# Performance work log

Hardware: AMD Instinct MI355X
Metric: run time of the kernel (lower is better)

The kernel has to match this reference:

```python
import jax, jax.numpy as jnp
import numpy as np
import math

B, S, D = 2, 2048, 1024
H = 16
HD = D // H
FFN = 2048
E = 8
TOP_K = 2
CAP_FACTOR = 1.25
EPS = 1e-6
BASE = 10000.0
CAP = max(math.ceil(B * S * TOP_K * CAP_FACTOR / E), 1)  # 1280


def setup_inputs() -> dict:
    key = jax.random.key(0)
    ks = jax.random.split(key, 6)
    sd = 0.02
    return {
        "x": jax.random.normal(ks[0], (B, S, D), jnp.float32),
        "g1": jnp.ones((D,), jnp.float32),
        "w_qkv": jax.random.normal(ks[1], (D, 3 * D), jnp.float32) * sd,
        "w_o": jax.random.normal(ks[2], (D, D), jnp.float32) * sd,
        "g2": jnp.ones((D,), jnp.float32),
        "w_router": jax.random.normal(ks[3], (D, E), jnp.float32) * sd,
        "w1": jax.random.normal(ks[4], (E, D, FFN), jnp.float32) * sd,
        "w2": jax.random.normal(ks[5], (E, FFN, D), jnp.float32) * sd,
    }


def _rmsnorm(x, w):
    rms = jax.lax.rsqrt(jnp.mean(x * x, axis=-1, keepdims=True) + EPS)
    return w * x * rms


def _rope(x, cos, sin):
    # x: [b,h,s,hd]; consecutive pairs (2i, 2i+1) form complex numbers
    xr = x[..., 0::2]
    xi = x[..., 1::2]
    c = cos[None, None]  # [1,1,s,hd/2]
    s_ = sin[None, None]
    out_r = xr * c - xi * s_
    out_i = xr * s_ + xi * c
    return jnp.stack([out_r, out_i], axis=-1).reshape(x.shape)


def _mha(x, w_qkv, w_o):
    b, s, d = x.shape
    qkv = x @ w_qkv
    q, k, v = jnp.split(qkv, 3, axis=-1)
    to_heads = lambda z: z.reshape(b, s, H, HD).transpose(0, 2, 1, 3)
    q, k, v = to_heads(q), to_heads(k), to_heads(v)
    # rotary embedding
    theta = BASE ** (-2.0 * (jnp.arange(HD // 2, dtype=jnp.float32) / HD))
    freqs = jnp.arange(s, dtype=jnp.float32)[:, None] * theta[None, :]  # [s,hd/2]
    cos, sin = jnp.cos(freqs), jnp.sin(freqs)
    q = _rope(q, cos, sin)
    k = _rope(k, cos, sin)
    scores = jnp.einsum('bhqd,bhkd->bhqk', q, k) / jnp.sqrt(jnp.float32(HD))
    causal = jnp.tril(jnp.ones((s, s), dtype=bool))
    scores = jnp.where(causal, scores, -jnp.inf)
    attn = jax.nn.softmax(scores, axis=-1)
    y = jnp.einsum('bhqk,bhkd->bhqd', attn, v)
    y = y.transpose(0, 2, 1, 3).reshape(b, s, d)
    return y @ w_o


def _moe(x, w_router, w1, w2):
    b, s, d = x.shape
    t = b * s
    xf = x.reshape(t, d)
    logits = xf.astype(jnp.float32) @ w_router.astype(jnp.float32)
    probs = jax.nn.softmax(logits, axis=-1)  # [t,E]
    g, eidx = jax.lax.top_k(probs, TOP_K)  # [t,K]
    fg = g.reshape(t * TOP_K)
    fe = eidx.reshape(t * TOP_K)
    tok_of = jnp.arange(t * TOP_K) // TOP_K
    # per-expert masked gates, then capacity-based top-CAP selection
    masked = jnp.where(fe[None, :] == jnp.arange(E)[:, None], fg[None, :], -jnp.inf)  # [E, t*K]
    vals, idx = jax.lax.top_k(masked, CAP)  # [E, CAP]
    valid = jnp.isfinite(vals)
    gates = jnp.where(valid, vals, 0.0)  # dropped/empty slots get zero gate
    tok = tok_of[idx]  # [E, CAP] token ids (arbitrary for invalid slots, gate 0)
    xe = xf[tok]  # [E, CAP, d]
    h = jax.nn.relu(jnp.einsum('ecd,edf->ecf', xe, w1))
    ye = jnp.einsum('ecf,efd->ecd', h, w2) * gates[..., None]
    y = jnp.zeros_like(xf).at[tok.reshape(-1)].add(ye.reshape(-1, d))
    return y.reshape(b, s, d)


def reference(x, g1, w_qkv, w_o, g2, w_router, w1, w2):
    x = x + _mha(_rmsnorm(x, g1), w_qkv, w_o)
    x = x + _moe(_rmsnorm(x, g2), w_router, w1, w2)
    return x
```

## Files before the change

kernel.cpp:

```cpp
#include <hip/hip_runtime.h>
#include <math.h>


#define B_   2
#define S_   2048
#define D_   1024
#define H_   16
#define HD_  64
#define FFN_ 2048
#define E_   8
#define CAP_ 1280
#define T_   (B_*S_)

typedef unsigned short u16;
typedef __attribute__((ext_vector_type(8))) short     short8;
typedef __attribute__((ext_vector_type(8))) _Float16  half8;
typedef __attribute__((ext_vector_type(8))) unsigned short ushort8v;
typedef __attribute__((ext_vector_type(4))) float     f32x4;

__device__ __forceinline__ u16 f2bf(float f) {
  unsigned u = __float_as_uint(f);
  return (u16)((u + 0x7fffu + ((u >> 16) & 1u)) >> 16);
}
__device__ __forceinline__ float bf2f(u16 h) {
  return __uint_as_float(((unsigned)h) << 16);
}
__device__ __forceinline__ u16 f2h(float f) {
  _Float16 h = (_Float16)f;
  return __builtin_bit_cast(u16, h);
}
__device__ __forceinline__ float h2f(u16 b) {
  return (float)__builtin_bit_cast(_Float16, b);
}

__device__ __forceinline__ void cstore(float* p, float v) { *p = v; }
__device__ __forceinline__ void cstore(u16* p, float v)   { *p = f2bf(v); }

__device__ __forceinline__ void glds16(const u16* g, u16* l) {
  __builtin_amdgcn_global_load_lds(
      (const __attribute__((address_space(1))) unsigned int*)g,
      (__attribute__((address_space(3))) unsigned int*)l, 16, 0, 0);
}

__global__ void init_k(int* cnt) {
  if (threadIdx.x < 16) cnt[threadIdx.x] = 0;
}

__global__ __launch_bounds__(256) void rmsnorm_k(const float* __restrict__ x,
                                                 const float* __restrict__ g,
                                                 float* __restrict__ of,
                                                 u16*   __restrict__ ob,
                                                 u16*   __restrict__ ohh,
                                                 u16*   __restrict__ ohl) {
  const int t = blockIdx.x, tid = threadIdx.x;
  const float4 xv = ((const float4*)(x + (size_t)t * D_))[tid];
  float ss = xv.x*xv.x + xv.y*xv.y + xv.z*xv.z + xv.w*xv.w;
  #pragma unroll
  for (int off = 32; off; off >>= 1) ss += __shfl_down(ss, off);
  __shared__ float wsum[4];
  if ((tid & 63) == 0) wsum[tid >> 6] = ss;
  __syncthreads();
  const float tot = wsum[0] + wsum[1] + wsum[2] + wsum[3];
  const float rms = 1.0f / sqrtf(tot * (1.0f / D_) + 1e-6f);
  const float4 gv = ((const float4*)g)[tid];
  float4 o;
  o.x = gv.x * xv.x * rms;
  o.y = gv.y * xv.y * rms;
  o.z = gv.z * xv.z * rms;
  o.w = gv.w * xv.w * rms;
  if (of) ((float4*)(of + (size_t)t * D_))[tid] = o;
  if (ob) {
    ushort4 h;
    h.x = f2bf(o.x); h.y = f2bf(o.y); h.z = f2bf(o.z); h.w = f2bf(o.w);
    ((ushort4*)(ob + (size_t)t * D_))[tid] = h;
  }
  if (ohh) {
    ushort4 hh, hl;
    hh.x = f2h(o.x); hl.x = f2h(o.x - h2f(hh.x));
    hh.y = f2h(o.y); hl.y = f2h(o.y - h2f(hh.y));
    hh.z = f2h(o.z); hl.z = f2h(o.z - h2f(hh.z));
    hh.w = f2h(o.w); hl.w = f2h(o.w - h2f(hh.w));
    ((ushort4*)(ohh + (size_t)t * D_))[tid] = hh;
    ((ushort4*)(ohl + (size_t)t * D_))[tid] = hl;
  }
}

template<bool RESID>
__global__ __launch_bounds__(256) void gemm_split(const u16* __restrict__ Ah,
                                                  const u16* __restrict__ Al,
                                                  const u16* __restrict__ Bh,
                                                  const u16* __restrict__ Bl,
                                                  const float* __restrict__ resid,
                                                  float* __restrict__ C,
                                                  int K, int lda, int ldb, int ldc) {
  __shared__ u16 AsH[128 * 32], AsL[128 * 32];
  __shared__ u16 BsH[128 * 32], BsL[128 * 32];
  const int tid = threadIdx.x;
  const int bm = blockIdx.y, bn = blockIdx.x;
  const int lane = tid & 63, wave = tid >> 6;
  const int wy = wave >> 1, wx = wave & 1;
  const int l15 = lane & 15, lq = lane >> 4;
  f32x4 acc[4][4];
  #pragma unroll
  for (int i = 0; i < 4; ++i)
    #pragma unroll
    for (int j = 0; j < 4; ++j)
      #pragma unroll
      for (int r = 0; r < 4; ++r) acc[i][j][r] = 0.0f;
  const int srow = lane >> 2, skc = (lane & 3) * 8;
  size_t ga[2], gb[2];
  int ldsoff[2];
  #pragma unroll
  for (int c = 0; c < 2; ++c) {
    const int q = wave * 2 + c;
    ga[c] = (size_t)(bm * 128 + q * 16 + srow) * lda + skc;
    gb[c] = (size_t)(bn * 128 + q * 16 + srow) * ldb + skc;
    ldsoff[c] = q * 512 + lane * 8;
  }

  for (int kt = 0; kt < K; kt += 32) {
    __syncthreads();
    #pragma unroll
    for (int c = 0; c < 2; ++c) {
      glds16(Ah + ga[c] + kt, &AsH[ldsoff[c]]);
      glds16(Al + ga[c] + kt, &AsL[ldsoff[c]]);
      glds16(Bh + gb[c] + kt, &BsH[ldsoff[c]]);
      glds16(Bl + gb[c] + kt, &BsL[ldsoff[c]]);
    }
    __syncthreads();
    half8 ah[4], al[4], bh[4], bl[4];
    #pragma unroll
    for (int i = 0; i < 4; ++i) {
      const int row = (wy * 64 + i * 16 + l15) * 32 + lq * 8;
      ah[i] = *(const half8*)&AsH[row];
      al[i] = *(const half8*)&AsL[row];
    }
    #pragma unroll
    for (int j = 0; j < 4; ++j) {
      const int row = (wx * 64 + j * 16 + l15) * 32 + lq * 8;
      bh[j] = *(const half8*)&BsH[row];
      bl[j] = *(const half8*)&BsL[row];
    }
    #pragma unroll
    for (int i = 0; i < 4; ++i)
      #pragma unroll
      for (int j = 0; j < 4; ++j) {
        acc[i][j] = __builtin_amdgcn_mfma_f32_16x16x32_f16(ah[i], bh[j], acc[i][j], 0, 0, 0);
        acc[i][j] = __builtin_amdgcn_mfma_f32_16x16x32_f16(ah[i], bl[j], acc[i][j], 0, 0, 0);
        acc[i][j] = __builtin_amdgcn_mfma_f32_16x16x32_f16(al[i], bh[j], acc[i][j], 0, 0, 0);
      }
  }
  #pragma unroll
  for (int i = 0; i < 4; ++i)
    #pragma unroll
    for (int j = 0; j < 4; ++j)
      #pragma unroll
      for (int r = 0; r < 4; ++r) {
        const int row = bm * 128 + wy * 64 + i * 16 + lq * 4 + r;
        const int col = bn * 128 + wx * 64 + j * 16 + l15;
        float v = acc[i][j][r];
        if (RESID) v += resid[(size_t)row * ldc + col];
        C[(size_t)row * ldc + col] = v;
      }
}

__global__ __launch_bounds__(256) void wsplit_t_k(const float* __restrict__ src,
                                                  u16* __restrict__ dh,
                                                  u16* __restrict__ dl,
                                                  int R, int C) {
  __shared__ float tile[32][33];
  const int tid = threadIdx.x;
  const int r0 = blockIdx.y * 32, c0 = blockIdx.x * 32;
  const int tx = tid & 31, ty = tid >> 5;
  #pragma unroll
  for (int i = 0; i < 4; ++i)
    tile[ty + i * 8][tx] = src[(size_t)(r0 + ty + i * 8) * C + c0 + tx];
  __syncthreads();
  #pragma unroll
  for (int i = 0; i < 4; ++i) {
    const float v = tile[tx][ty + i * 8];
    const u16 hh = f2h(v);
    const size_t o = (size_t)(c0 + ty + i * 8) * R + r0 + tx;
    dh[o] = hh;
    dl[o] = f2h(v - h2f(hh));
  }
}

__global__ __launch_bounds__(256) void ropesplit_k(const float* __restrict__ qkv,
                                                   u16* __restrict__ qhi, u16* __restrict__ qlo,
                                                   u16* __restrict__ khi, u16* __restrict__ klo) {
  const int i = blockIdx.x * 256 + threadIdx.x;
  const int j = i & 31;
  const int h = (i >> 5) & 15;
  const int t = i >> 9;
  const int s = t & (S_ - 1);
  const int b = t >> 11;
  const int bh = b * 16 + h;
  const float theta = (float)pow(10000.0, -(double)j / 32.0);
  const float fr = (float)s * theta;
  const float c = cosf(fr), sn = sinf(fr);
  const float2 q = *(const float2*)(qkv + (size_t)t * 3072 + h * 64 + 2 * j);
  const float2 k = *(const float2*)(qkv + (size_t)t * 3072 + 1024 + h * 64 + 2 * j);
  const float q0 = (q.x * c - q.y * sn) * 0.125f;
  const float q1 = (q.x * sn + q.y * c) * 0.125f;
  const float k0 = k.x * c - k.y * sn;
  const float k1 = k.x * sn + k.y * c;
  const size_t o = ((size_t)bh * S_ + s) * 32 + j;
  const u16 qh0 = f2bf(q0), qh1 = f2bf(q1);
  const u16 kh0 = f2bf(k0), kh1 = f2bf(k1);
  ((unsigned*)qhi)[o] = (unsigned)qh0 | ((unsigned)qh1 << 16);
  ((unsigned*)khi)[o] = (unsigned)kh0 | ((unsigned)kh1 << 16);
  const u16 ql0 = f2bf(q0 - bf2f(qh0)), ql1 = f2bf(q1 - bf2f(qh1));
  const u16 kl0 = f2bf(k0 - bf2f(kh0)), kl1 = f2bf(k1 - bf2f(kh1));
  ((unsigned*)qlo)[o] = (unsigned)ql0 | ((unsigned)ql1 << 16);
  ((unsigned*)klo)[o] = (unsigned)kl0 | ((unsigned)kl1 << 16);
}

__global__ __launch_bounds__(256) void vsplit_k(const float* __restrict__ qkv,
                                                u16* __restrict__ vthi,
                                                u16* __restrict__ vtlo) {
  __shared__ float tile[64][65];
  const int st = blockIdx.x, bh = blockIdx.y;
  const int b = bh >> 4, h = bh & 15;
  const int tid = threadIdx.x;
  const int c = tid & 63, r4 = tid >> 6;
  #pragma unroll
  for (int i = 0; i < 16; ++i) {
    const int r = i * 4 + r4;
    tile[r][c] = qkv[(size_t)(b * S_ + st * 64 + r) * 3072 + 2048 + h * 64 + c];
  }
  __syncthreads();
  #pragma unroll
  for (int i = 0; i < 16; ++i) {
    const int d = i * 4 + r4;
    const float v = tile[c][d];
    const u16 hi = f2bf(v);
    const size_t o = ((size_t)bh * 64 + d) * S_ + st * 64 + c;
    vthi[o] = hi;
    vtlo[o] = f2bf(v - bf2f(hi));
  }
}

__global__ __launch_bounds__(256) void attn_mfma_k(const u16* __restrict__ qhi,
                                                   const u16* __restrict__ qlo,
                                                   const u16* __restrict__ khi,
                                                   const u16* __restrict__ klo,
                                                   const u16* __restrict__ vthi,
                                                   const u16* __restrict__ vtlo,
                                                   u16* __restrict__ ahh,
                                                   u16* __restrict__ ahl,
                                                   float* __restrict__ PO,
                                                   float* __restrict__ Pm,
                                                   float* __restrict__ Pl2) {
  __shared__ u16 Kh[64 * 68], Kl[64 * 68];
  __shared__ u16 Vh[64 * 68], Vl[64 * 68];
  __shared__ u16 Ph[4][16 * 68], Pl[4][16 * 68];
  const int tid = threadIdx.x, lane = tid & 63, wave = tid >> 6;
  const int bi = blockIdx.x;
  int qt, k0, k1, chunk;
  bool partial;
  if (bi < 32) {
    qt = 31 - (bi >> 1); chunk = bi & 1;
    const int nk = qt + 1, cut = nk >> 1;
    k0 = chunk ? cut : 0;
    k1 = chunk ? nk : cut;
    partial = true;
  } else {
    qt = 47 - bi; chunk = 0; k0 = 0; k1 = qt + 1; partial = false;
  }
  const int bh = blockIdx.y;
  const int l15 = lane & 15, lq = lane >> 4;
  const size_t hb = (size_t)bh * S_ * 64;
  const int qrow = qt * 64 + wave * 16 + l15;
  short8 qh[2], ql[2];
  qh[0] = *(const short8*)(qhi + hb + (size_t)qrow * 64 + lq * 8);
  qh[1] = *(const short8*)(qhi + hb + (size_t)qrow * 64 + 32 + lq * 8);
  ql[0] = *(const short8*)(qlo + hb + (size_t)qrow * 64 + lq * 8);
  ql[1] = *(const short8*)(qlo + hb + (size_t)qrow * 64 + 32 + lq * 8);
  f32x4 O[4];
  float m_i[4], l_i[4];
  #pragma unroll
  for (int n = 0; n < 4; ++n)
    #pragma unroll
    for (int r = 0; r < 4; ++r) O[n][r] = 0.0f;
  #pragma unroll
  for (int r = 0; r < 4; ++r) { m_i[r] = -__builtin_inff(); l_i[r] = 0.0f; }

  for (int kt = k0; kt < k1; ++kt) {
    __syncthreads();
    #pragma unroll
    for (int it = 0; it < 2; ++it) {
      const int idx = it * 256 + tid;
      const int row = idx >> 3, c8 = (idx & 7) * 8;
      const size_t koff = hb + (size_t)(kt * 64 + row) * 64 + c8;
      *(ushort8v*)&Kh[row * 68 + c8] = *(const ushort8v*)(khi + koff);
      *(ushort8v*)&Kl[row * 68 + c8] = *(const ushort8v*)(klo + koff);
      const size_t voff = ((size_t)bh * 64 + row) * S_ + kt * 64 + c8;
      *(ushort8v*)&Vh[row * 68 + c8] = *(const ushort8v*)(vthi + voff);
      *(ushort8v*)&Vl[row * 68 + c8] = *(const ushort8v*)(vtlo + voff);
    }
    __syncthreads();
    f32x4 sc[4];
    #pragma unroll
    for (int n = 0; n < 4; ++n)
      #pragma unroll
      for (int r = 0; r < 4; ++r) sc[n][r] = 0.0f;
    #pragma unroll
    for (int n = 0; n < 4; ++n) {
      const int krow = (n * 16 + l15) * 68 + lq * 8;
      const short8 kb0 = *(const short8*)&Kh[krow];
      const short8 kb1 = *(const short8*)&Kh[krow + 32];
      const short8 kl0 = *(const short8*)&Kl[krow];
      const short8 kl1 = *(const short8*)&Kl[krow + 32];
      sc[n] = __builtin_amdgcn_mfma_f32_16x16x32_bf16(qh[0], kb0, sc[n], 0, 0, 0);
      sc[n] = __builtin_amdgcn_mfma_f32_16x16x32_bf16(qh[1], kb1, sc[n], 0, 0, 0);
      sc[n] = __builtin_amdgcn_mfma_f32_16x16x32_bf16(qh[0], kl0, sc[n], 0, 0, 0);
      sc[n] = __builtin_amdgcn_mfma_f32_16x16x32_bf16(qh[1], kl1, sc[n], 0, 0, 0);
      sc[n] = __builtin_amdgcn_mfma_f32_16x16x32_bf16(ql[0], kb0, sc[n], 0, 0, 0);
      sc[n] = __builtin_amdgcn_mfma_f32_16x16x32_bf16(ql[1], kb1, sc[n], 0, 0, 0);
    }
    if (kt == qt) {
      #pragma unroll
      for (int n = 0; n < 4; ++n)
        #pragma unroll
        for (int r = 0; r < 4; ++r)
          if (n * 16 + l15 > wave * 16 + lq * 4 + r) sc[n][r] = -__builtin_inff();
    }
    float al[4];
    #pragma unroll
    for (int r = 0; r < 4; ++r) {
      float mx = fmaxf(fmaxf(sc[0][r], sc[1][r]), fmaxf(sc[2][r], sc[3][r]));
      mx = fmaxf(mx, __shfl_xor(mx, 1));
      mx = fmaxf(mx, __shfl_xor(mx, 2));
      mx = fmaxf(mx, __shfl_xor(mx, 4));
      mx = fmaxf(mx, __shfl_xor(mx, 8));
      const float mn = fmaxf(m_i[r], mx);
      al[r] = __expf(m_i[r] - mn);
      m_i[r] = mn;
    }
    f32x4 p[4];
    #pragma unroll
    for (int n = 0; n < 4; ++n)
      #pragma unroll
      for (int r = 0; r < 4; ++r) p[n][r] = __expf(sc[n][r] - m_i[r]);
    #pragma unroll
    for (int r = 0; r < 4; ++r) {
      float rs = p[0][r] + p[1][r] + p[2][r] + p[3][r];
      rs += __shfl_xor(rs, 1);
      rs += __shfl_xor(rs, 2);
      rs += __shfl_xor(rs, 4);
      rs += __shfl_xor(rs, 8);
      l_i[r] = l_i[r] * al[r] + rs;
      O[0][r] *= al[r]; O[1][r] *= al[r]; O[2][r] *= al[r]; O[3][r] *= al[r];
    }
    #pragma unroll
    for (int n = 0; n < 4; ++n)
      #pragma unroll
      for (int r = 0; r < 4; ++r) {
        const float v = p[n][r];
        const u16 hi = f2bf(v);
        const int a = (lq * 4 + r) * 68 + n * 16 + l15;
        Ph[wave][a] = hi;
        Pl[wave][a] = f2bf(v - bf2f(hi));
      }
    asm volatile("s_waitcnt lgkmcnt(0)" ::: "memory");
    short8 pah[2], pal[2];
    pah[0] = *(const short8*)&Ph[wave][l15 * 68 + lq * 8];
    pah[1] = *(const short8*)&Ph[wave][l15 * 68 + 32 + lq * 8];
    pal[0] = *(const short8*)&Pl[wave][l15 * 68 + lq * 8];
    pal[1] = *(const short8*)&Pl[wave][l15 * 68 + 32 + lq * 8];
    #pragma unroll
    for (int n = 0; n < 4; ++n) {
      const int vrow = (n * 16 + l15) * 68 + lq * 8;
      const short8 vb0 = *(const short8*)&Vh[vrow];
      const short8 vb1 = *(const short8*)&Vh[vrow + 32];
      const short8 vl0 = *(const short8*)&Vl[vrow];
      const short8 vl1 = *(const short8*)&Vl[vrow + 32];
      O[n] = __builtin_amdgcn_mfma_f32_16x16x32_bf16(pah[0], vb0, O[n], 0, 0, 0);
      O[n] = __builtin_amdgcn_mfma_f32_16x16x32_bf16(pah[1], vb1, O[n], 0, 0, 0);
      O[n] = __builtin_amdgcn_mfma_f32_16x16x32_bf16(pah[0], vl0, O[n], 0, 0, 0);
      O[n] = __builtin_amdgcn_mfma_f32_16x16x32_bf16(pah[1], vl1, O[n], 0, 0, 0);
      O[n] = __builtin_amdgcn_mfma_f32_16x16x32_bf16(pal[0], vb0, O[n], 0, 0, 0);
      O[n] = __builtin_amdgcn_mfma_f32_16x16x32_bf16(pal[1], vb1, O[n], 0, 0, 0);
    }
  }
  const int b = bh >> 4, h = bh & 15;
  if (!partial) {
    #pragma unroll
    for (int r = 0; r < 4; ++r) {
      const float inv = 1.0f / l_i[r];
      const int row = qt * 64 + wave * 16 + lq * 4 + r;
      const size_t base = (size_t)(b * S_ + row) * D_ + h * 64 + l15;
      #pragma unroll
      for (int n = 0; n < 4; ++n) {
        const float o = O[n][r] * inv;
        const u16 hh = f2h(o);
        ahh[base + n * 16] = hh;
        ahl[base + n * 16] = f2h(o - h2f(hh));
      }
    }
  } else {
    #pragma unroll
    for (int r = 0; r < 4; ++r) {
      const int prow = qt * 64 + wave * 16 + lq * 4 + r - 1024;
      const size_t idx = (size_t)(chunk * 32 + bh) * 1024 + prow;
      float* po = PO + idx * 64;
      #pragma unroll
      for (int n = 0; n < 4; ++n) po[n * 16 + l15] = O[n][r];
      if (l15 == 0) { Pm[idx] = m_i[r]; Pl2[idx] = l_i[r]; }
    }
  }
}

__global__ __launch_bounds__(256) void attn_combine_k(const float* __restrict__ PO,
                                                      const float* __restrict__ Pm,
                                                      const float* __restrict__ Pl2,
                                                      u16* __restrict__ ahh,
                                                      u16* __restrict__ ahl) {
  const int tid = threadIdx.x;
  const int bh = blockIdx.y, b = bh >> 4, h = bh & 15;
  const int prow = blockIdx.x * 64 + (tid >> 2);
  const int d0 = (tid & 3) * 16;
  const size_t i0 = (size_t)bh * 1024 + prow;
  const size_t i1 = (size_t)(32 + bh) * 1024 + prow;
  const float m0 = Pm[i0], m1 = Pm[i1];
  const float M = fmaxf(m0, m1);
  const float w0 = __expf(m0 - M), w1 = __expf(m1 - M);
  const float inv = 1.0f / (w0 * Pl2[i0] + w1 * Pl2[i1]);
  const int row = 1024 + prow;
  const size_t ob = (size_t)(b * S_ + row) * D_ + h * 64 + d0;
  #pragma unroll
  for (int q4 = 0; q4 < 4; ++q4) {
    const float4 o0 = *(const float4*)(PO + i0 * 64 + d0 + q4 * 4);
    const float4 o1 = *(const float4*)(PO + i1 * 64 + d0 + q4 * 4);
    float v[4];
    v[0] = (w0 * o0.x + w1 * o1.x) * inv;
    v[1] = (w0 * o0.y + w1 * o1.y) * inv;
    v[2] = (w0 * o0.z + w1 * o1.z) * inv;
    v[3] = (w0 * o0.w + w1 * o1.w) * inv;
    ushort4 hh, hl;
    u16* ph = (u16*)&hh;
    u16* pl = (u16*)&hl;
    #pragma unroll
    for (int z = 0; z < 4; ++z) {
      ph[z] = f2h(v[z]);
      pl[z] = f2h(v[z] - h2f(ph[z]));
    }
    *(ushort4*)(ahh + ob + q4 * 4) = hh;
    *(ushort4*)(ahl + ob + q4 * 4) = hl;
  }
}

__global__ __launch_bounds__(256) void router_k(const float* __restrict__ y2,
                                                const float* __restrict__ wr,
                                                int*   __restrict__ cnt,
                                                int*   __restrict__ tok_e,
                                                float* __restrict__ tok_g,
                                                int*   __restrict__ tok_p,
                                                int*   __restrict__ etok) {
  const int wave = threadIdx.x >> 6, lane = threadIdx.x & 63;
  const int t = blockIdx.x * 4 + wave;
  const float* xr = y2 + (size_t)t * D_;
  float acc[8];
  #pragma unroll
  for (int e = 0; e < 8; ++e) acc[e] = 0.0f;
  for (int c = 0; c < 16; ++c) {
    const float xv = xr[c * 64 + lane];
    const float* w = wr + (size_t)(c * 64 + lane) * 8;
    #pragma unroll
    for (int e = 0; e < 8; ++e) acc[e] = fmaf(xv, w[e], acc[e]);
  }
  #pragma unroll
  for (int off = 32; off; off >>= 1)
    #pragma unroll
    for (int e = 0; e < 8; ++e) acc[e] += __shfl_down(acc[e], off);
  if (lane == 0) {
    float mx = acc[0];
    #pragma unroll
    for (int e = 1; e < 8; ++e) mx = fmaxf(mx, acc[e]);
    float ex[8], sum = 0.0f;
    #pragma unroll
    for (int e = 0; e < 8; ++e) { ex[e] = expf(acc[e] - mx); sum += ex[e]; }
    int e1 = 0;
    #pragma unroll
    for (int e = 1; e < 8; ++e) if (acc[e] > acc[e1]) e1 = e;
    int e2 = (e1 == 0) ? 1 : 0;
    #pragma unroll
    for (int e = 0; e < 8; ++e) if (e != e1 && acc[e] > acc[e2]) e2 = e;
    const float g1v = ex[e1] / sum, g2v = ex[e2] / sum;
    int p1 = atomicAdd(&cnt[e1], 1);
    int p2 = atomicAdd(&cnt[e2], 1);
    if (p1 < CAP_) etok[e1 * CAP_ + p1] = t; else p1 = -1;
    if (p2 < CAP_) etok[e2 * CAP_ + p2] = t; else p2 = -1;
    tok_e[2*t] = e1;   tok_e[2*t+1] = e2;
    tok_g[2*t] = g1v;  tok_g[2*t+1] = g2v;
    tok_p[2*t] = p1;   tok_p[2*t+1] = p2;
  }
}

__global__ __launch_bounds__(256) void gather_k(const u16* __restrict__ y2b,
                                                const int* __restrict__ etok,
                                                const int* __restrict__ cnt,
                                                u16* __restrict__ xe) {
  const int e = blockIdx.y, pos = blockIdx.x, tid = threadIdx.x;
  const int n = min(cnt[e], CAP_);
  ushort4* dst = (ushort4*)(xe + (size_t)(e * CAP_ + pos) * D_) + tid;
  if (pos < n) {
    const int t = etok[e * CAP_ + pos];
    *dst = ((const ushort4*)(y2b + (size_t)t * D_))[tid];
  } else {
    *dst = make_ushort4(0, 0, 0, 0);
  }
}

template<typename OT, bool RELU>
__global__ __launch_bounds__(256) void gemm_bt(const u16* __restrict__ A,
                                               const u16* __restrict__ Bt,
                                               OT* __restrict__ C,
                                               int M, int N, int K,
                                               int lda, int ldb, int ldc,
                                               long sAz, long sBz, long sCz) {
  __shared__ u16 As[128 * 32];
  __shared__ u16 Bs[128 * 32];
  const int tid = threadIdx.x;
  A  += (size_t)blockIdx.z * sAz;
  Bt += (size_t)blockIdx.z * sBz;
  C  += (size_t)blockIdx.z * sCz;
  const int bm = blockIdx.y, bn = blockIdx.x;
  const int lane = tid & 63, wave = tid >> 6;
  const int wy = wave >> 1, wx = wave & 1;
  const int l15 = lane & 15, lq = lane >> 4;
  f32x4 acc[4][4];
  #pragma unroll
  for (int i = 0; i < 4; ++i)
    #pragma unroll
    for (int j = 0; j < 4; ++j)
      #pragma unroll
      for (int r = 0; r < 4; ++r) acc[i][j][r] = 0.0f;
  const int srow = lane >> 2, skc = (lane & 3) * 8;
  size_t ga[2], gb[2];
  int ldsoff[2];
  #pragma unroll
  for (int c = 0; c < 2; ++c) {
    const int q = wave * 2 + c;
    ga[c] = (size_t)(bm * 128 + q * 16 + srow) * lda + skc;
    gb[c] = (size_t)(bn * 128 + q * 16 + srow) * ldb + skc;
    ldsoff[c] = q * 512 + lane * 8;
  }

  for (int kt = 0; kt < K; kt += 32) {
    __syncthreads();
    #pragma unroll
    for (int c = 0; c < 2; ++c) {
      glds16(A  + ga[c] + kt, &As[ldsoff[c]]);
      glds16(Bt + gb[c] + kt, &Bs[ldsoff[c]]);
    }
    __syncthreads();
    short8 a[4], b[4];
    #pragma unroll
    for (int i = 0; i < 4; ++i)
      a[i] = *(const short8*)&As[(wy * 64 + i * 16 + l15) * 32 + lq * 8];
    #pragma unroll
    for (int j = 0; j < 4; ++j)
      b[j] = *(const short8*)&Bs[(wx * 64 + j * 16 + l15) * 32 + lq * 8];
    #pragma unroll
    for (int i = 0; i < 4; ++i)
      #pragma unroll
      for (int j = 0; j < 4; ++j)
        acc[i][j] = __builtin_amdgcn_mfma_f32_16x16x32_bf16(a[i], b[j], acc[i][j], 0, 0, 0);
  }
  #pragma unroll
  for (int i = 0; i < 4; ++i)
    #pragma unroll
    for (int j = 0; j < 4; ++j)
      #pragma unroll
      for (int r = 0; r < 4; ++r) {
        const int row = bm * 128 + wy * 64 + i * 16 + lq * 4 + r;
        const int col = bn * 128 + wx * 64 + j * 16 + l15;
        float v = acc[i][j][r];
        if (RELU) v = fmaxf(v, 0.0f);
        cstore(C + (size_t)row * ldc + col, v);
      }
}

__global__ __launch_bounds__(256) void transpose_bf_k(const float* __restrict__ src,
                                                      u16* __restrict__ dst,
                                                      int R, int C) {
  __shared__ float tile[32][33];
  const int tid = threadIdx.x;
  const size_t zoff = (size_t)blockIdx.z * R * C;
  const int r0 = blockIdx.y * 32, c0 = blockIdx.x * 32;
  const int tx = tid & 31, ty = tid >> 5;
  #pragma unroll
  for (int i = 0; i < 4; ++i)
    tile[ty + i * 8][tx] = src[zoff + (size_t)(r0 + ty + i * 8) * C + c0 + tx];
  __syncthreads();
  #pragma unroll
  for (int i = 0; i < 4; ++i)
    dst[zoff + (size_t)(c0 + ty + i * 8) * R + r0 + tx] = f2bf(tile[tx][ty + i * 8]);
}

__global__ __launch_bounds__(256) void combine_k(const float* __restrict__ x2,
                                                 const float* __restrict__ ye,
                                                 const int*   __restrict__ tok_e,
                                                 const float* __restrict__ tok_g,
                                                 const int*   __restrict__ tok_p,
                                                 float* __restrict__ out) {
  const int t = blockIdx.x, tid = threadIdx.x;
  float4 v = ((const float4*)(x2 + (size_t)t * D_))[tid];
  #pragma unroll
  for (int r = 0; r < 2; ++r) {
    const int p = tok_p[2 * t + r];
    if (p >= 0) {
      const int e = tok_e[2 * t + r];
      const float g = tok_g[2 * t + r];
      const float4 y = ((const float4*)(ye + (size_t)(e * CAP_ + p) * D_))[tid];
      v.x = fmaf(g, y.x, v.x);
      v.y = fmaf(g, y.y, v.y);
      v.z = fmaf(g, y.z, v.z);
      v.w = fmaf(g, y.w, v.w);
    }
  }
  ((float4*)(out + (size_t)t * D_))[tid] = v;
}

extern "C" void kernel_launch(void* const* d_in, const int* in_sizes, int n_in,
                              void* d_out, int out_size, void* d_ws, size_t ws_size,
                              hipStream_t stream) {
  const float* x    = (const float*)d_in[0];
  const float* g1   = (const float*)d_in[1];
  const float* wqkv = (const float*)d_in[2];
  const float* wo   = (const float*)d_in[3];
  const float* g2   = (const float*)d_in[4];
  const float* wr   = (const float*)d_in[5];
  const float* w1   = (const float*)d_in[6];
  const float* w2   = (const float*)d_in[7];
  float* out = (float*)d_out;
  char* ws = (char*)d_ws;
  const size_t MB = 1ull << 20;

  u16*   y1hh  = (u16*)  (ws + 0);
  u16*   y1hl  = (u16*)  (ws + 8 * MB);
  u16*   ahh   = (u16*)  (ws + 16 * MB);
  u16*   ahl   = (u16*)  (ws + 24 * MB);
  u16*   hbf   = (u16*)  (ws + 0);
  float* qkv   = (float*)(ws + 40 * MB);
  float* PO    = (float*)(ws + 40 * MB);
  float* Pm    = (float*)(ws + 58 * MB);
  float* Pl2   = (float*)(ws + 59 * MB);
  u16*   xe    = (u16*)  (ws + 40 * MB);
  float* x2    = (float*)(ws + 88 * MB);
  float* y2    = (float*)(ws + 104 * MB);
  u16*   y2b   = (u16*)  (ws + 120 * MB);
  u16*   w1t   = (u16*)  (ws + 128 * MB);
  u16*   w2t   = (u16*)  (ws + 160 * MB);
  float* ye    = (float*)(ws + 192 * MB);
  u16*   wqh   = (u16*)  (ws + 192 * MB);
  u16*   wql   = (u16*)  (ws + 198 * MB);
  u16*   khi   = (u16*)  (ws + 192 * MB);
  u16*   klo   = (u16*)  (ws + 200 * MB);
  u16*   vthi  = (u16*)  (ws + 208 * MB);
  u16*   vtlo  = (u16*)  (ws + 216 * MB);
  u16*   woh   = (u16*)  (ws + 224 * MB);
  u16*   wol   = (u16*)  (ws + 226 * MB);
  int*   cnt   = (int*)  (ws + 232 * MB);
  int*   tok_e = cnt + 16;
  float* tok_g = (float*)(tok_e + 2 * T_);
  int*   tok_p = (int*)  (tok_g + 2 * T_);
  int*   etok  = tok_p + 2 * T_;

  init_k<<<1, 64, 0, stream>>>(cnt);
  transpose_bf_k<<<dim3(FFN_/32, D_/32, E_), 256, 0, stream>>>(w1, w1t, D_, FFN_);
  transpose_bf_k<<<dim3(D_/32, FFN_/32, E_), 256, 0, stream>>>(w2, w2t, FFN_, D_);
  wsplit_t_k<<<dim3(3*D_/32, D_/32), 256, 0, stream>>>(wqkv, wqh, wql, D_, 3*D_);
  wsplit_t_k<<<dim3(D_/32, D_/32), 256, 0, stream>>>(wo, woh, wol, D_, D_);

  rmsnorm_k<<<T_, 256, 0, stream>>>(x, g1, (float*)nullptr, (u16*)nullptr, y1hh, y1hl);
  gemm_split<false><<<dim3(3 * D_ / 128, T_ / 128), 256, 0, stream>>>(
      y1hh, y1hl, wqh, wql, nullptr, qkv, D_, D_, D_, 3 * D_);
  ropesplit_k<<<T_ * H_ * 32 / 256, 256, 0, stream>>>(qkv, y1hh, y1hl, khi, klo);
  vsplit_k<<<dim3(S_ / 64, B_ * H_), 256, 0, stream>>>(qkv, vthi, vtlo);
  attn_mfma_k<<<dim3(48, B_ * H_), 256, 0, stream>>>(
      y1hh, y1hl, khi, klo, vthi, vtlo, ahh, ahl, PO, Pm, Pl2);
  attn_combine_k<<<dim3(16, B_ * H_), 256, 0, stream>>>(PO, Pm, Pl2, ahh, ahl);
  gemm_split<true><<<dim3(D_ / 128, T_ / 128), 256, 0, stream>>>(
      ahh, ahl, woh, wol, x, x2, D_, D_, D_, D_);
  rmsnorm_k<<<T_, 256, 0, stream>>>(x2, g2, y2, y2b, (u16*)nullptr, (u16*)nullptr);
  router_k<<<T_ / 4, 256, 0, stream>>>(y2, wr, cnt, tok_e, tok_g, tok_p, etok);
  gather_k<<<dim3(CAP_, E_), 256, 0, stream>>>(y2b, etok, cnt, xe);
  gemm_bt<u16, true><<<dim3(FFN_/128, CAP_/128, E_), 256, 0, stream>>>(
      xe, w1t, hbf, CAP_, FFN_, D_, D_, D_, FFN_,
      (long)CAP_ * D_, (long)FFN_ * D_, (long)CAP_ * FFN_);
  gemm_bt<float, false><<<dim3(D_/128, CAP_/128, E_), 256, 0, stream>>>(
      hbf, w2t, ye, CAP_, D_, FFN_, FFN_, FFN_, D_,
      (long)CAP_ * FFN_, (long)D_ * FFN_, (long)CAP_ * D_);
  combine_k<<<T_, 256, 0, stream>>>(x2, ye, tok_e, tok_g, tok_p, out);
}
```

Measured before the change: 793.8 us.

## Keep attention P in registers via transposed QK^T and fp16 MFMA-packed V

The score MFMA operands are swapped so each lane holds a query column of S^T. That makes the row softmax a per-lane reduction with only two cross-lane shuffles, and lets the probabilities feed the PV MFMA directly as fp16 A-operands without a round trip through LDS. V is pre-packed by a new kernel into an MFMA-fragment-ordered hi/lo fp16 layout and loaded into LDS with direct global-to-LDS copies (glds16). This removes the P LDS store/reload, the separate Vh/Vl tiles and a waitcnt, and cuts LDS use. In exchange, P and V use a split-fp16 instead of split-bf16 representation, with the precision and range differences that brings, and the per-row m/l values now need shuffles at output.

```diff
diff --git a/kernel.cpp b/kernel.cpp
--- a/kernel.cpp
+++ b/kernel.cpp
@@ -15,6 +15,7 @@
 typedef unsigned short u16;
 typedef __attribute__((ext_vector_type(8))) short     short8;
 typedef __attribute__((ext_vector_type(8))) _Float16  half8;
+typedef __attribute__((ext_vector_type(4))) _Float16  half4;
 typedef __attribute__((ext_vector_type(8))) unsigned short ushort8v;
 typedef __attribute__((ext_vector_type(4))) float     f32x4;
 
@@ -216,28 +217,28 @@
   ((unsigned*)klo)[o] = (unsigned)kl0 | ((unsigned)kl1 << 16);
 }
 
-__global__ __launch_bounds__(256) void vsplit_k(const float* __restrict__ qkv,
-                                                u16* __restrict__ vthi,
-                                                u16* __restrict__ vtlo) {
-  __shared__ float tile[64][65];
-  const int st = blockIdx.x, bh = blockIdx.y;
+__global__ __launch_bounds__(256) void vpack_k(const float* __restrict__ qkv,
+                                               u16* __restrict__ vpk) {
+  const int kt = blockIdx.x, bh = blockIdx.y;
   const int b = bh >> 4, h = bh & 15;
   const int tid = threadIdx.x;
-  const int c = tid & 63, r4 = tid >> 6;
-  #pragma unroll
-  for (int i = 0; i < 16; ++i) {
-    const int r = i * 4 + r4;
-    tile[r][c] = qkv[(size_t)(b * S_ + st * 64 + r) * 3072 + 2048 + h * 64 + c];
-  }
-  __syncthreads();
-  #pragma unroll
-  for (int i = 0; i < 16; ++i) {
-    const int d = i * 4 + r4;
-    const float v = tile[c][d];
-    const u16 hi = f2bf(v);
-    const size_t o = ((size_t)bh * 64 + d) * S_ + st * 64 + c;
-    vthi[o] = hi;
-    vtlo[o] = f2bf(v - bf2f(hi));
+  u16* dst = vpk + (size_t)(bh * 32 + kt) * 8192;
+  #pragma unroll
+  for (int i = 0; i < 4; ++i) {
+    const int g = i * 256 + tid;
+    const int lane = g & 63, n = (g >> 6) & 3, kc = g >> 8;
+    const int lq = lane >> 4, l15 = lane & 15;
+    const int key = kt * 64 + kc * 16 + lq * 4;
+    const int d = n * 16 + l15;
+    u16 out[8];
+    #pragma unroll
+    for (int j = 0; j < 4; ++j) {
+      const float v = qkv[(size_t)(b * S_ + key + j) * 3072 + 2048 + h * 64 + d];
+      const u16 hh = f2h(v);
+      out[j] = hh;
+      out[4 + j] = f2h(v - h2f(hh));
+    }
+    *(ushort8v*)(dst + g * 8) = *(ushort8v*)out;
   }
 }
 
@@ -245,16 +246,14 @@
                                                    const u16* __restrict__ qlo,
                                                    const u16* __restrict__ khi,
                                                    const u16* __restrict__ klo,
-                                                   const u16* __restrict__ vthi,
-                                                   const u16* __restrict__ vtlo,
+                                                   const u16* __restrict__ vpk,
                                                    u16* __restrict__ ahh,
                                                    u16* __restrict__ ahl,
                                                    float* __restrict__ PO,
                                                    float* __restrict__ Pm,
                                                    float* __restrict__ Pl2) {
   __shared__ u16 Kh[64 * 68], Kl[64 * 68];
-  __shared__ u16 Vh[64 * 68], Vl[64 * 68];
-  __shared__ u16 Ph[4][16 * 68], Pl[4][16 * 68];
+  __shared__ u16 Vp[8192];
   const int tid = threadIdx.x, lane = tid & 63, wave = tid >> 6;
   const int bi = blockIdx.x;
   int qt, k0, k1, chunk;
@@ -278,16 +277,20 @@
   ql[0] = *(const short8*)(qlo + hb + (size_t)qrow * 64 + lq * 8);
   ql[1] = *(const short8*)(qlo + hb + (size_t)qrow * 64 + 32 + lq * 8);
   f32x4 O[4];
-  float m_i[4], l_i[4];
   #pragma unroll
   for (int n = 0; n < 4; ++n)
     #pragma unroll
     for (int r = 0; r < 4; ++r) O[n][r] = 0.0f;
-  #pragma unroll
-  for (int r = 0; r < 4; ++r) { m_i[r] = -__builtin_inff(); l_i[r] = 0.0f; }
+  float m_i = -__builtin_inff(), l_i = 0.0f;
 
   for (int kt = k0; kt < k1; ++kt) {
     __syncthreads();
+    {
+      const u16* vg = vpk + (size_t)(bh * 32 + kt) * 8192 + wave * 2048;
+      #pragma unroll
+      for (int c = 0; c < 4; ++c)
+        glds16(vg + c * 512 + lane * 8, &Vp[wave * 2048 + c * 512 + lane * 8]);
+    }
     #pragma unroll
     for (int it = 0; it < 2; ++it) {
       const int idx = it * 256 + tid;
@@ -295,100 +298,86 @@
       const size_t koff = hb + (size_t)(kt * 64 + row) * 64 + c8;
       *(ushort8v*)&Kh[row * 68 + c8] = *(const ushort8v*)(khi + koff);
       *(ushort8v*)&Kl[row * 68 + c8] = *(const ushort8v*)(klo + koff);
-      const size_t voff = ((size_t)bh * 64 + row) * S_ + kt * 64 + c8;
-      *(ushort8v*)&Vh[row * 68 + c8] = *(const ushort8v*)(vthi + voff);
-      *(ushort8v*)&Vl[row * 68 + c8] = *(const ushort8v*)(vtlo + voff);
     }
     __syncthreads();
     f32x4 sc[4];
     #pragma unroll
-    for (int n = 0; n < 4; ++n)
-      #pragma unroll
-      for (int r = 0; r < 4; ++r) sc[n][r] = 0.0f;
-    #pragma unroll
-    for (int n = 0; n < 4; ++n) {
-      const int krow = (n * 16 + l15) * 68 + lq * 8;
+    for (int kc = 0; kc < 4; ++kc)
+      #pragma unroll
+      for (int r = 0; r < 4; ++r) sc[kc][r] = 0.0f;
+    #pragma unroll
+    for (int kc = 0; kc < 4; ++kc) {
+      const int krow = (kc * 16 + l15) * 68 + lq * 8;
       const short8 kb0 = *(const short8*)&Kh[krow];
       const short8 kb1 = *(const short8*)&Kh[krow + 32];
       const short8 kl0 = *(const short8*)&Kl[krow];
       const short8 kl1 = *(const short8*)&Kl[krow + 32];
-      sc[n] = __builtin_amdgcn_mfma_f32_16x16x32_bf16(qh[0], kb0, sc[n], 0, 0, 0);
-      sc[n] = __builtin_amdgcn_mfma_f32_16x16x32_bf16(qh[1], kb1, sc[n], 0, 0, 0);
-      sc[n] = __builtin_amdgcn_mfma_f32_16x16x32_bf16(qh[0], kl0, sc[n], 0, 0, 0);
-      sc[n] = __builtin_amdgcn_mfma_f32_16x16x32_bf16(qh[1], kl1, sc[n], 0, 0, 0);
-      sc[n] = __builtin_amdgcn_mfma_f32_16x16x32_bf16(ql[0], kb0, sc[n], 0, 0, 0);
-      sc[n] = __builtin_amdgcn_mfma_f32_16x16x32_bf16(ql[1], kb1, sc[n], 0, 0, 0);
+      sc[kc] = __builtin_amdgcn_mfma_f32_16x16x32_bf16(kb0, qh[0], sc[kc], 0, 0, 0);
+      sc[kc] = __builtin_amdgcn_mfma_f32_16x16x32_bf16(kb1, qh[1], sc[kc], 0, 0, 0);
+      sc[kc] = __builtin_amdgcn_mfma_f32_16x16x32_bf16(kb0, ql[0], sc[kc], 0, 0, 0);
+      sc[kc] = __builtin_amdgcn_mfma_f32_16x16x32_bf16(kb1, ql[1], sc[kc], 0, 0, 0);
+      sc[kc] = __builtin_amdgcn_mfma_f32_16x16x32_bf16(kl0, qh[0], sc[kc], 0, 0, 0);
+      sc[kc] = __builtin_amdgcn_mfma_f32_16x16x32_bf16(kl1, qh[1], sc[kc], 0, 0, 0);
     }
     if (kt == qt) {
       #pragma unroll
-      for (int n = 0; n < 4; ++n)
+      for (int kc = 0; kc < 4; ++kc)
         #pragma unroll
         for (int r = 0; r < 4; ++r)
-          if (n * 16 + l15 > wave * 16 + lq * 4 + r) sc[n][r] = -__builtin_inff();
-    }
-    float al[4];
+          if (kc * 16 + lq * 4 + r > wave * 16 + l15) sc[kc][r] = -__builtin_inff();
+    }
+    float mx = -__builtin_inff();
+    #pragma unroll
+    for (int kc = 0; kc < 4; ++kc)
+      #pragma unroll
+      for (int r = 0; r < 4; ++r) mx = fmaxf(mx, sc[kc][r]);
+    mx = fmaxf(mx, __shfl_xor(mx, 16));
+    mx = fmaxf(mx, __shfl_xor(mx, 32));
+    const float mn = fmaxf(m_i, mx);
+    const float alpha = __expf(m_i - mn);
+    m_i = mn;
+    f32x4 p[4];
+    float rs = 0.0f;
+    #pragma unroll
+    for (int kc = 0; kc < 4; ++kc)
+      #pragma unroll
+      for (int r = 0; r < 4; ++r) { p[kc][r] = __expf(sc[kc][r] - m_i); rs += p[kc][r]; }
+    rs += __shfl_xor(rs, 16);
+    rs += __shfl_xor(rs, 32);
+    l_i = l_i * alpha + rs;
     #pragma unroll
     for (int r = 0; r < 4; ++r) {
-      float mx = fmaxf(fmaxf(sc[0][r], sc[1][r]), fmaxf(sc[2][r], sc[3][r]));
-      mx = fmaxf(mx, __shfl_xor(mx, 1));
-      mx = fmaxf(mx, __shfl_xor(mx, 2));
-      mx = fmaxf(mx, __shfl_xor(mx, 4));
-      mx = fmaxf(mx, __shfl_xor(mx, 8));
-      const float mn = fmaxf(m_i[r], mx);
-      al[r] = __expf(m_i[r] - mn);
-      m_i[r] = mn;
-    }
-    f32x4 p[4];
+      const float alr = __shfl(alpha, lq * 4 + r);
+      #pragma unroll
+      for (int n = 0; n < 4; ++n) O[n][r] *= alr;
+    }
+    half4 ph[4], pl[4];
+    #pragma unroll
+    for (int kc = 0; kc < 4; ++kc)
+      #pragma unroll
+      for (int r = 0; r < 4; ++r) {
+        const _Float16 hi = (_Float16)p[kc][r];
+        ph[kc][r] = hi;
+        pl[kc][r] = (_Float16)(p[kc][r] - (float)hi);
+      }
     #pragma unroll
     for (int n = 0; n < 4; ++n)
       #pragma unroll
-      for (int r = 0; r < 4; ++r) p[n][r] = __expf(sc[n][r] - m_i[r]);
-    #pragma unroll
-    for (int r = 0; r < 4; ++r) {
-      float rs = p[0][r] + p[1][r] + p[2][r] + p[3][r];
-      rs += __shfl_xor(rs, 1);
-      rs += __shfl_xor(rs, 2);
-      rs += __shfl_xor(rs, 4);
-      rs += __shfl_xor(rs, 8);
-      l_i[r] = l_i[r] * al[r] + rs;
-      O[0][r] *= al[r]; O[1][r] *= al[r]; O[2][r] *= al[r]; O[3][r] *= al[r];
-    }
-    #pragma unroll
-    for (int n = 0; n < 4; ++n)
-      #pragma unroll
-      for (int r = 0; r < 4; ++r) {
-        const float v = p[n][r];
-        const u16 hi = f2bf(v);
-        const int a = (lq * 4 + r) * 68 + n * 16 + l15;
-        Ph[wave][a] = hi;
-        Pl[wave][a] = f2bf(v - bf2f(hi));
+      for (int kc = 0; kc < 4; ++kc) {
+        const int g = ((kc * 4 + n) * 64 + lane) * 8;
+        const half4 vh = *(const half4*)&Vp[g];
+        const half4 vl = *(const half4*)&Vp[g + 4];
+        O[n] = __builtin_amdgcn_mfma_f32_16x16x16f16(ph[kc], vh, O[n], 0, 0, 0);
+        O[n] = __builtin_amdgcn_mfma_f32_16x16x16f16(ph[kc], vl, O[n], 0, 0, 0);
+        O[n] = __builtin_amdgcn_mfma_f32_16x16x16f16(pl[kc], vh, O[n], 0, 0, 0);
       }
-    asm volatile("s_waitcnt lgkmcnt(0)" ::: "memory");
-    short8 pah[2], pal[2];
-    pah[0] = *(const short8*)&Ph[wave][l15 * 68 + lq * 8];
-    pah[1] = *(const short8*)&Ph[wave][l15 * 68 + 32 + lq * 8];
-    pal[0] = *(const short8*)&Pl[wave][l15 * 68 + lq * 8];
-    pal[1] = *(const short8*)&Pl[wave][l15 * 68 + 32 + lq * 8];
-    #pragma unroll
-    for (int n = 0; n < 4; ++n) {
-      const int vrow = (n * 16 + l15) * 68 + lq * 8;
-      const short8 vb0 = *(const short8*)&Vh[vrow];
-      const short8 vb1 = *(const short8*)&Vh[vrow + 32];
-      const short8 vl0 = *(const short8*)&Vl[vrow];
-      const short8 vl1 = *(const short8*)&Vl[vrow + 32];
-      O[n] = __builtin_amdgcn_mfma_f32_16x16x32_bf16(pah[0], vb0, O[n], 0, 0, 0);
-      O[n] = __builtin_amdgcn_mfma_f32_16x16x32_bf16(pah[1], vb1, O[n], 0, 0, 0);
-      O[n] = __builtin_amdgcn_mfma_f32_16x16x32_bf16(pah[0], vl0, O[n], 0, 0, 0);
-      O[n] = __builtin_amdgcn_mfma_f32_16x16x32_bf16(pah[1], vl1, O[n], 0, 0, 0);
-      O[n] = __builtin_amdgcn_mfma_f32_16x16x32_bf16(pal[0], vb0, O[n], 0, 0, 0);
-      O[n] = __builtin_amdgcn_mfma_f32_16x16x32_bf16(pal[1], vb1, O[n], 0, 0, 0);
-    }
   }
   const int b = bh >> 4, h = bh & 15;
   if (!partial) {
     #pragma unroll
     for (int r = 0; r < 4; ++r) {
-      const float inv = 1.0f / l_i[r];
+      const float lr = __shfl(l_i, lq * 4 + r);
+      const float inv = 1.0f / lr;
       const int row = qt * 64 + wave * 16 + lq * 4 + r;
       const size_t base = (size_t)(b * S_ + row) * D_ + h * 64 + l15;
       #pragma unroll
@@ -407,7 +396,11 @@
       float* po = PO + idx * 64;
       #pragma unroll
       for (int n = 0; n < 4; ++n) po[n * 16 + l15] = O[n][r];
-      if (l15 == 0) { Pm[idx] = m_i[r]; Pl2[idx] = l_i[r]; }
+    }
+    if (lq == 0) {
+      const int prow = qt * 64 + wave * 16 + l15 - 1024;
+      const size_t idx = (size_t)(chunk * 32 + bh) * 1024 + prow;
+      Pm[idx] = m_i; Pl2[idx] = l_i;
     }
   }
 }
@@ -659,8 +652,7 @@
   u16*   wql   = (u16*)  (ws + 198 * MB);
   u16*   khi   = (u16*)  (ws + 192 * MB);
   u16*   klo   = (u16*)  (ws + 200 * MB);
-  u16*   vthi  = (u16*)  (ws + 208 * MB);
-  u16*   vtlo  = (u16*)  (ws + 216 * MB);
+  u16*   vpk   = (u16*)  (ws + 208 * MB);
   u16*   woh   = (u16*)  (ws + 224 * MB);
   u16*   wol   = (u16*)  (ws + 226 * MB);
   int*   cnt   = (int*)  (ws + 232 * MB);
@@ -679,9 +671,9 @@
   gemm_split<false><<<dim3(3 * D_ / 128, T_ / 128), 256, 0, stream>>>(
       y1hh, y1hl, wqh, wql, nullptr, qkv, D_, D_, D_, 3 * D_);
   ropesplit_k<<<T_ * H_ * 32 / 256, 256, 0, stream>>>(qkv, y1hh, y1hl, khi, klo);
-  vsplit_k<<<dim3(S_ / 64, B_ * H_), 256, 0, stream>>>(qkv, vthi, vtlo);
+  vpack_k<<<dim3(S_ / 64, B_ * H_), 256, 0, stream>>>(qkv, vpk);
   attn_mfma_k<<<dim3(48, B_ * H_), 256, 0, stream>>>(
-      y1hh, y1hl, khi, klo, vthi, vtlo, ahh, ahl, PO, Pm, Pl2);
+      y1hh, y1hl, khi, klo, vpk, ahh, ahl, PO, Pm, Pl2);
   attn_combine_k<<<dim3(16, B_ * H_), 256, 0, stream>>>(PO, Pm, Pl2, ahh, ahl);
   gemm_split<true><<<dim3(D_ / 128, T_ / 128), 256, 0, stream>>>(
       ahh, ahl, woh, wol, x, x2, D_, D_, D_, D_);
```

After: 747.1 us. 1.06x faster.
